# Kernel optimization log

Hardware: AMD Instinct MI355X
Metric: run time of the kernel (lower is better)

Reference implementation:

```python
import jax, jax.numpy as jnp
import numpy as np

B, H, L, D = 4, 8, 2048, 64
FACTOR = 5


def setup_inputs() -> dict:
    key = jax.random.key(0)
    kq, kk, kv, ki = jax.random.split(key, 4)
    sample_k = min(FACTOR * int(np.ceil(np.log(L))), L)  # = 40
    queries = jax.random.normal(kq, (B, H, L, D), jnp.float32)
    keys = jax.random.normal(kk, (B, H, L, D), jnp.float32)
    values = jax.random.normal(kv, (B, H, L, D), jnp.float32)
    index_sample = jax.random.randint(ki, (L, sample_k), 0, L)
    return {"queries": queries, "keys": keys, "values": values,
            "index_sample": index_sample}


def prob_attention(queries, keys, values, index_sample):
    Bq, Hq, L_Q, Dk = queries.shape
    L_K = keys.shape[2]
    n_top = min(FACTOR * int(np.ceil(np.log(L_Q))), L_Q)  # u
    scale = float(1.0 / np.sqrt(Dk))

    # --- _prob_QK: sample scores for each query over random key subset ---
    # K_sample: (B,H,L_Q,S,D); index_sample shared across batch/heads
    K_sample = keys[:, :, index_sample, :]
    Q_K_sample = jnp.einsum('bhld,bhlsd->bhls', queries, K_sample)
    # sparsity measure M = max - mean (mean over full L_K as in source)
    M = Q_K_sample.max(-1) - Q_K_sample.sum(-1) / L_K      # (B,H,L_Q)
    M_top = jax.lax.top_k(M, n_top)[1]                     # (B,H,u) query indices

    # full scores only for the selected "active" queries
    Q_reduce = jnp.take_along_axis(queries, M_top[..., None], axis=2)  # (B,H,u,D)
    scores = jnp.einsum('bhud,bhkd->bhuk', Q_reduce, keys) * scale     # (B,H,u,L_K)

    # --- causal ProbMask: key j masked when j > selected query position ---
    causal = jnp.arange(L_K)[None, None, None, :] > M_top[..., None]
    scores = jnp.where(causal, -jnp.inf, scores)
    attn = jax.nn.softmax(scores, axis=-1)
    ctx_update = jnp.einsum('bhuk,bhkd->bhud', attn, values)           # (B,H,u,D)

    # --- initial context (causal branch): running cumulative sum of V ---
    context = jnp.cumsum(values, axis=2)                               # (B,H,L_Q,D)

    # scatter active-query results back into the context
    b_idx = jnp.arange(Bq)[:, None, None]
    h_idx = jnp.arange(Hq)[None, :, None]
    context = context.at[b_idx, h_idx, M_top].set(ctx_update)
    return context


def reference(queries, keys, values, index_sample):
    return prob_attention(queries, keys, values, index_sample)
```

## Files before the change

### kernel.cpp

```cpp
#include <hip/hip_runtime.h>
#include <hip/hip_bf16.h>
#include <cstdint>

#define BB 4
#define HH 8
#define LL 2048
#define DD 64
#define SK 40
#define NT 40
#define BHN (BB*HH)
#define SCALE 0.125f
#define CHUNK 128
#define NCH (LL/CHUNK)

#define WS_M    0
#define WS_SUB  (WS_M + BHN*LL)
#define WS_CTX  (WS_SUB + BHN*64*DD)
#define WS_PM   (WS_CTX + BHN*NT*DD)
#define WS_PSUM (WS_PM + BHN*NT*NCH)
#define WS_PACC (WS_PSUM + BHN*NT*NCH)
#define WS_TOP  (WS_PACC + BHN*NT*NCH*DD)

__global__ __launch_bounds__(256) void k1_M(const float* __restrict__ Q,
                                            const float* __restrict__ K,
                                            const int* __restrict__ isamp,
                                            float* __restrict__ M) {
    int wid  = blockIdx.x * 4 + (threadIdx.x >> 6);
    int lane = threadIdx.x & 63;
    int bh   = wid >> 11;
    int l    = wid & (LL - 1);
    int g    = lane >> 4;
    int e    = lane & 15;

    float4 q = reinterpret_cast<const float4*>(Q + (size_t)wid * DD)[e];

    const float* Kbh = K + (size_t)bh * LL * DD;
    const int* irow = isamp + l * SK;

    float mx = -INFINITY, sm = 0.f;
#pragma unroll
    for (int p = 0; p < SK / 4; p++) {
        int s = p * 4 + g;
        int idx = irow[s];
        float4 kv = reinterpret_cast<const float4*>(Kbh + (size_t)idx * DD)[e];
        float d = q.x * kv.x + q.y * kv.y + q.z * kv.z + q.w * kv.w;
        d += __shfl_xor(d, 1);
        d += __shfl_xor(d, 2);
        d += __shfl_xor(d, 4);
        d += __shfl_xor(d, 8);
        mx = fmaxf(mx, d);
        sm += d;
    }
    mx = fmaxf(mx, __shfl_xor(mx, 16));
    mx = fmaxf(mx, __shfl_xor(mx, 32));
    sm += __shfl_xor(sm, 16);
    sm += __shfl_xor(sm, 32);
    if (lane == 0) M[wid] = mx - sm * (1.0f / (float)LL);
}

__global__ __launch_bounds__(64) void k2_topk(const float* __restrict__ M,
                                              int* __restrict__ Mtop) {
    __shared__ float m_lds[LL];
    int bh = blockIdx.x, lane = threadIdx.x;
    for (int i = lane; i < LL; i += 64) m_lds[i] = M[bh * LL + i];
    __syncthreads();
    for (int t = 0; t < NT; t++) {
        unsigned long long best = 0ull;
#pragma unroll
        for (int j = 0; j < LL / 64; j++) {
            int i = lane + j * 64;
            float v = m_lds[i];
            unsigned u = __float_as_uint(v);
            u = (u & 0x80000000u) ? ~u : (u | 0x80000000u);
            unsigned long long key = ((unsigned long long)u << 32) | (unsigned)(~i);
            if (key > best) best = key;
        }
#pragma unroll
        for (int off = 32; off; off >>= 1) {
            unsigned long long o = __shfl_xor(best, off);
            if (o > best) best = o;
        }
        int idx = (int)(~(unsigned)(best & 0xFFFFFFFFull));
        if (lane == 0) {
            Mtop[bh * NT + t] = idx;
            m_lds[idx] = -INFINITY;
        }
        __syncthreads();
    }
}

__global__ __launch_bounds__(256) void k3a_partial(const float* __restrict__ Q,
                                                   const float* __restrict__ K,
                                                   const float* __restrict__ V,
                                                   const int* __restrict__ Mtop,
                                                   float* __restrict__ pm,
                                                   float* __restrict__ psum,
                                                   float* __restrict__ pacc) {
    __shared__ float q_lds[NT * DD];
    __shared__ float s_lds[NT][CHUNK];
    __shared__ int   qi_lds[NT];
    int bh = blockIdx.x / NCH;
    int ch = blockIdx.x % NCH;
    int ck = ch * CHUNK;
    int tid = threadIdx.x;

    if (tid < NT) qi_lds[tid] = Mtop[bh * NT + tid];
    __syncthreads();
    for (int c = tid; c < NT * 16; c += 256) {
        int u = c >> 4, j = c & 15;
        reinterpret_cast<float4*>(q_lds)[c] =
            reinterpret_cast<const float4*>(Q + ((size_t)bh * LL + qi_lds[u]) * DD)[j];
    }
    __syncthreads();

    int k   = ck + (tid >> 1);
    int half = tid & 1;
    const float4* krow = reinterpret_cast<const float4*>(K + ((size_t)bh * LL + k) * DD) + half * 8;
    float4 kreg[8];
#pragma unroll
    for (int j = 0; j < 8; j++) kreg[j] = krow[j];
    for (int u = 0; u < NT; u++) {
        const float4* q4 = reinterpret_cast<const float4*>(q_lds + u * DD) + half * 8;
        float d = 0.f;
#pragma unroll
        for (int j = 0; j < 8; j++) {
            float4 a = q4[j], b = kreg[j];
            d += a.x * b.x + a.y * b.y + a.z * b.z + a.w * b.w;
        }
        d += __shfl_xor(d, 1);
        float s = (k <= qi_lds[u]) ? d * SCALE : -INFINITY;
        if (half == 0) s_lds[u][k - ck] = s;
    }
    __syncthreads();

    int w = tid >> 6, lane = tid & 63;
#pragma unroll
    for (int uu = 0; uu < NT / 4; uu++) {
        int u = w + uu * 4;
        float s0 = s_lds[u][lane], s1 = s_lds[u][lane + 64];
        float m = fmaxf(s0, s1);
#pragma unroll
        for (int off = 32; off; off >>= 1) m = fmaxf(m, __shfl_xor(m, off));
        float e0 = (s0 == -INFINITY) ? 0.f : __expf(s0 - m);
        float e1 = (s1 == -INFINITY) ? 0.f : __expf(s1 - m);
        s_lds[u][lane] = e0;
        s_lds[u][lane + 64] = e1;
        float sm = e0 + e1;
#pragma unroll
        for (int off = 32; off; off >>= 1) sm += __shfl_xor(sm, off);
        if (lane == 0) {
            pm  [((size_t)bh * NT + u) * NCH + ch] = m;
            psum[((size_t)bh * NT + u) * NCH + ch] = sm;
        }
    }
    __syncthreads();

    float acc[NT / 4] = {};
    const float* vbase = V + ((size_t)bh * LL + ck) * DD + lane;
#pragma unroll 4
    for (int kk = 0; kk < CHUNK; kk++) {
        float v = vbase[(size_t)kk * DD];
#pragma unroll
        for (int uu = 0; uu < NT / 4; uu++)
            acc[uu] += s_lds[w + uu * 4][kk] * v;
    }
#pragma unroll
    for (int uu = 0; uu < NT / 4; uu++) {
        int u = w + uu * 4;
        pacc[(((size_t)bh * NT + u) * NCH + ch) * DD + lane] = acc[uu];
    }
}

__global__ __launch_bounds__(64) void k3b_reduce(const float* __restrict__ pm,
                                                 const float* __restrict__ psum,
                                                 const float* __restrict__ pacc,
                                                 float* __restrict__ ctx) {
    int row = blockIdx.x;
    int lane = threadIdx.x;
    float pmv[NCH];
    float m = -INFINITY;
#pragma unroll
    for (int i = 0; i < NCH; i++) {
        pmv[i] = pm[(size_t)row * NCH + i];
        m = fmaxf(m, pmv[i]);
    }
    float Z = 0.f, acc = 0.f;
#pragma unroll
    for (int i = 0; i < NCH; i++) {
        float sc = (pmv[i] == -INFINITY) ? 0.f : __expf(pmv[i] - m);
        Z   += psum[(size_t)row * NCH + i] * sc;
        acc += pacc[((size_t)row * NCH + i) * DD + lane] * sc;
    }
    ctx[(size_t)row * DD + lane] = acc / Z;
}

__global__ __launch_bounds__(64) void k4a_sub(const float* __restrict__ V,
                                              float* __restrict__ sub) {
    int blk = blockIdx.x;
    int lane = threadIdx.x;
    size_t base = (size_t)blk * 32 * DD + lane;
    float acc = 0.f;
#pragma unroll 8
    for (int r = 0; r < 32; r++) acc += V[base + (size_t)r * DD];
    sub[(size_t)blk * DD + lane] = acc;
}

__global__ __launch_bounds__(64) void k4b_scan(const float* __restrict__ V,
                                               const float* __restrict__ sub,
                                               float* __restrict__ out) {
    int blk = blockIdx.x;
    int bh = blk >> 6, j = blk & 63;
    int lane = threadIdx.x;
    float off = 0.f;
    for (int p = 0; p < j; p++) off += sub[((size_t)(bh * 64 + p)) * DD + lane];
    size_t base = (size_t)blk * 32 * DD + lane;
    float acc = off;
    for (int r = 0; r < 32; r++) {
        acc += V[base + (size_t)r * DD];
        out[base + (size_t)r * DD] = acc;
    }
}

__global__ __launch_bounds__(256) void k5_scatter(const int* __restrict__ Mtop,
                                                  const float* __restrict__ ctx,
                                                  float* __restrict__ out) {
    int bh = blockIdx.x, tid = threadIdx.x;
    for (int t = tid; t < NT * DD; t += 256) {
        int u = t >> 6, d = t & 63;
        int row = Mtop[bh * NT + u];
        out[((size_t)bh * LL + row) * DD + d] = ctx[((size_t)bh * NT + u) * DD + d];
    }
}

extern "C" void kernel_launch(void* const* d_in, const int* in_sizes, int n_in,
                              void* d_out, int out_size, void* d_ws, size_t ws_size,
                              hipStream_t stream) {
    const float* Q = (const float*)d_in[0];
    const float* K = (const float*)d_in[1];
    const float* V = (const float*)d_in[2];
    const int* isamp = (const int*)d_in[3];
    float* ws   = (float*)d_ws;
    float* M    = ws + WS_M;
    float* sub  = ws + WS_SUB;
    float* ctx  = ws + WS_CTX;
    float* pm   = ws + WS_PM;
    float* psum = ws + WS_PSUM;
    float* pacc = ws + WS_PACC;
    int*   Mtop = (int*)(ws + WS_TOP);
    float* out  = (float*)d_out;

    k1_M      <<<BHN * LL / 4, 256, 0, stream>>>(Q, K, isamp, M);
    k2_topk   <<<BHN,           64, 0, stream>>>(M, Mtop);
    k3a_partial<<<BHN * NCH,   256, 0, stream>>>(Q, K, V, Mtop, pm, psum, pacc);
    k3b_reduce<<<BHN * NT,      64, 0, stream>>>(pm, psum, pacc, ctx);
    k4a_sub   <<<BHN * 64,      64, 0, stream>>>(V, sub);
    k4b_scan  <<<BHN * 64,      64, 0, stream>>>(V, sub, out);
    k5_scatter<<<BHN,          256, 0, stream>>>(Mtop, ctx, out);
}
```

Before: 214.9 us.

## Register-resident top-k, XCD block swizzle, fuse reduce with scatter

The top-k kernel now keeps all 2048 sortable keys in registers per lane and knocks out the previous winner each round, removing LDS traffic and the per-iteration barrier. k1 and k3a remap block indices so neighbouring work lands on the same XCD (group of 8), which should improve L2 locality for K reuse. The softmax partial reduce is fused with the scatter into the output, dropping the ctx buffer and one launch. The register-resident keys (32 x 64-bit per lane) raise register pressure in the top-k kernel.

```diff
diff --git a/kernel.cpp b/kernel.cpp
--- a/kernel.cpp
+++ b/kernel.cpp
@@ -25,7 +25,9 @@
                                             const float* __restrict__ K,
                                             const int* __restrict__ isamp,
                                             float* __restrict__ M) {
-    int wid  = blockIdx.x * 4 + (threadIdx.x >> 6);
+    int bid  = blockIdx.x;
+    int swz  = (bid & 7) * (BHN * LL / 4 / 8) + (bid >> 3);
+    int wid  = swz * 4 + (threadIdx.x >> 6);
     int lane = threadIdx.x & 63;
     int bh   = wid >> 11;
     int l    = wid & (LL - 1);
@@ -60,32 +62,33 @@
 
 __global__ __launch_bounds__(64) void k2_topk(const float* __restrict__ M,
                                               int* __restrict__ Mtop) {
-    __shared__ float m_lds[LL];
     int bh = blockIdx.x, lane = threadIdx.x;
-    for (int i = lane; i < LL; i += 64) m_lds[i] = M[bh * LL + i];
-    __syncthreads();
+    const float* Mb = M + (size_t)bh * LL;
+    unsigned long long key[32];
+#pragma unroll
+    for (int j = 0; j < 32; j++) {
+        int i = lane + j * 64;
+        unsigned u = __float_as_uint(Mb[i]);
+        u = (u & 0x80000000u) ? ~u : (u | 0x80000000u);
+        key[j] = ((unsigned long long)u << 32) | (unsigned)(~i);
+    }
+    unsigned long long winner = 0ull;
     for (int t = 0; t < NT; t++) {
         unsigned long long best = 0ull;
 #pragma unroll
-        for (int j = 0; j < LL / 64; j++) {
-            int i = lane + j * 64;
-            float v = m_lds[i];
-            unsigned u = __float_as_uint(v);
-            u = (u & 0x80000000u) ? ~u : (u | 0x80000000u);
-            unsigned long long key = ((unsigned long long)u << 32) | (unsigned)(~i);
-            if (key > best) best = key;
+        for (int j = 0; j < 32; j++) {
+            unsigned long long k = key[j];
+            k = (k == winner) ? 0ull : k;
+            key[j] = k;
+            best = (k > best) ? k : best;
         }
 #pragma unroll
         for (int off = 32; off; off >>= 1) {
             unsigned long long o = __shfl_xor(best, off);
-            if (o > best) best = o;
-        }
-        int idx = (int)(~(unsigned)(best & 0xFFFFFFFFull));
-        if (lane == 0) {
-            Mtop[bh * NT + t] = idx;
-            m_lds[idx] = -INFINITY;
-        }
-        __syncthreads();
+            best = (o > best) ? o : best;
+        }
+        winner = best;
+        if (lane == 0) Mtop[bh * NT + t] = (int)(~(unsigned)(best & 0xFFFFFFFFull));
     }
 }
 
@@ -99,8 +102,10 @@
     __shared__ float q_lds[NT * DD];
     __shared__ float s_lds[NT][CHUNK];
     __shared__ int   qi_lds[NT];
-    int bh = blockIdx.x / NCH;
-    int ch = blockIdx.x % NCH;
+    int bid = blockIdx.x;
+    int swz = (bid & 7) * (BHN * NCH / 8) + (bid >> 3);
+    int bh = swz / NCH;
+    int ch = swz % NCH;
     int ck = ch * CHUNK;
     int tid = threadIdx.x;
 
@@ -169,29 +174,6 @@
         int u = w + uu * 4;
         pacc[(((size_t)bh * NT + u) * NCH + ch) * DD + lane] = acc[uu];
     }
-}
-
-__global__ __launch_bounds__(64) void k3b_reduce(const float* __restrict__ pm,
-                                                 const float* __restrict__ psum,
-                                                 const float* __restrict__ pacc,
-                                                 float* __restrict__ ctx) {
-    int row = blockIdx.x;
-    int lane = threadIdx.x;
-    float pmv[NCH];
-    float m = -INFINITY;
-#pragma unroll
-    for (int i = 0; i < NCH; i++) {
-        pmv[i] = pm[(size_t)row * NCH + i];
-        m = fmaxf(m, pmv[i]);
-    }
-    float Z = 0.f, acc = 0.f;
-#pragma unroll
-    for (int i = 0; i < NCH; i++) {
-        float sc = (pmv[i] == -INFINITY) ? 0.f : __expf(pmv[i] - m);
-        Z   += psum[(size_t)row * NCH + i] * sc;
-        acc += pacc[((size_t)row * NCH + i) * DD + lane] * sc;
-    }
-    ctx[(size_t)row * DD + lane] = acc / Z;
 }
 
 __global__ __launch_bounds__(64) void k4a_sub(const float* __restrict__ V,
@@ -221,15 +203,30 @@
     }
 }
 
-__global__ __launch_bounds__(256) void k5_scatter(const int* __restrict__ Mtop,
-                                                  const float* __restrict__ ctx,
+__global__ __launch_bounds__(64) void k3b_scatter(const float* __restrict__ pm,
+                                                  const float* __restrict__ psum,
+                                                  const float* __restrict__ pacc,
+                                                  const int* __restrict__ Mtop,
                                                   float* __restrict__ out) {
-    int bh = blockIdx.x, tid = threadIdx.x;
-    for (int t = tid; t < NT * DD; t += 256) {
-        int u = t >> 6, d = t & 63;
-        int row = Mtop[bh * NT + u];
-        out[((size_t)bh * LL + row) * DD + d] = ctx[((size_t)bh * NT + u) * DD + d];
-    }
+    int row = blockIdx.x;
+    int lane = threadIdx.x;
+    int bh = row / NT;
+    float pmv[NCH];
+    float m = -INFINITY;
+#pragma unroll
+    for (int i = 0; i < NCH; i++) {
+        pmv[i] = pm[(size_t)row * NCH + i];
+        m = fmaxf(m, pmv[i]);
+    }
+    float Z = 0.f, acc = 0.f;
+#pragma unroll
+    for (int i = 0; i < NCH; i++) {
+        float sc = (pmv[i] == -INFINITY) ? 0.f : __expf(pmv[i] - m);
+        Z   += psum[(size_t)row * NCH + i] * sc;
+        acc += pacc[((size_t)row * NCH + i) * DD + lane] * sc;
+    }
+    int qi = Mtop[row];
+    out[((size_t)bh * LL + qi) * DD + lane] = acc / Z;
 }
 
 extern "C" void kernel_launch(void* const* d_in, const int* in_sizes, int n_in,
@@ -242,18 +239,16 @@
     float* ws   = (float*)d_ws;
     float* M    = ws + WS_M;
     float* sub  = ws + WS_SUB;
-    float* ctx  = ws + WS_CTX;
     float* pm   = ws + WS_PM;
     float* psum = ws + WS_PSUM;
     float* pacc = ws + WS_PACC;
     int*   Mtop = (int*)(ws + WS_TOP);
     float* out  = (float*)d_out;
 
-    k1_M      <<<BHN * LL / 4, 256, 0, stream>>>(Q, K, isamp, M);
-    k2_topk   <<<BHN,           64, 0, stream>>>(M, Mtop);
-    k3a_partial<<<BHN * NCH,   256, 0, stream>>>(Q, K, V, Mtop, pm, psum, pacc);
-    k3b_reduce<<<BHN * NT,      64, 0, stream>>>(pm, psum, pacc, ctx);
-    k4a_sub   <<<BHN * 64,      64, 0, stream>>>(V, sub);
-    k4b_scan  <<<BHN * 64,      64, 0, stream>>>(V, sub, out);
-    k5_scatter<<<BHN,          256, 0, stream>>>(Mtop, ctx, out);
-}
+    k1_M       <<<BHN * LL / 4, 256, 0, stream>>>(Q, K, isamp, M);
+    k2_topk    <<<BHN,           64, 0, stream>>>(M, Mtop);
+    k3a_partial<<<BHN * NCH,    256, 0, stream>>>(Q, K, V, Mtop, pm, psum, pacc);
+    k4a_sub    <<<BHN * 64,      64, 0, stream>>>(V, sub);
+    k4b_scan   <<<BHN * 64,      64, 0, stream>>>(V, sub, out);
+    k3b_scatter<<<BHN * NT,      64, 0, stream>>>(pm, psum, pacc, Mtop, out);
+}
```

New measurement: 207.3 us. -3.5%, faster.
